# Optimization experiments

Measured on AMD Instinct MI355X. Metric: run time of the kernel, lower is better.

## Reference

```python
import jax, jax.numpy as jnp
import numpy as np

N = 2048; E = 5; C = 2; W_IN = 256; W_OUT = 128; NUM_CLASS = 8; NT = 1024


def _norm(H, add):
    # faithful to GTN.norm: transpose, zero diagonal, (optionally add I),
    # row-degree-normalize (diag(deg^-1) @ H expressed as row scaling), transpose back
    Ht = H.T
    n = Ht.shape[0]
    eye = jnp.eye(n, dtype=Ht.dtype)
    Ht = Ht * (1.0 - eye)
    if add:
        Ht = Ht + eye
    deg = jnp.sum(Ht, axis=1)
    deg_inv = jnp.where(deg == 0, jnp.zeros_like(deg), 1.0 / deg)
    return (deg_inv[:, None] * Ht).T


def _gtconv(A_e, w):
    # A_e: [E, N, N]; w: [C, E]; softmax over edge types then weighted sum
    return jnp.einsum('ce,enm->cnm', jax.nn.softmax(w, axis=1), A_e)


def setup_inputs() -> dict:
    key = jax.random.key(0)
    ks = jax.random.split(key, 12)
    A = jax.random.uniform(ks[0], (N, N, E), dtype=jnp.float32)
    X = jax.random.uniform(ks[1], (N, W_IN), dtype=jnp.float32)  # BCE target, in [0,1]
    target_x = jax.random.randint(ks[2], (NT,), 0, N)
    target = jax.random.randint(ks[3], (NT,), 0, NUM_CLASS)
    w0a = 0.1 * jax.random.normal(ks[4], (C, E), dtype=jnp.float32)
    w0b = 0.1 * jax.random.normal(ks[5], (C, E), dtype=jnp.float32)
    w1a = 0.1 * jax.random.normal(ks[6], (C, E), dtype=jnp.float32)
    W = jax.random.normal(ks[7], (W_IN, W_OUT), dtype=jnp.float32) * (1.0 / np.sqrt(W_IN))
    W1 = jax.random.normal(ks[8], (W_OUT * C, W_OUT), dtype=jnp.float32) * (1.0 / np.sqrt(W_OUT * C))
    W2 = jax.random.normal(ks[9], (W_OUT * C, W_IN), dtype=jnp.float32) * (1.0 / np.sqrt(W_OUT * C))
    lin_w = jax.random.normal(ks[10], (NUM_CLASS, W_OUT), dtype=jnp.float32) * (1.0 / np.sqrt(W_OUT))
    lin_b = jnp.zeros((NUM_CLASS,), dtype=jnp.float32)
    return {"A": A, "X": X, "W": W, "W1": W1, "W2": W2, "lin_w": lin_w,
            "lin_b": lin_b, "w0a": w0a, "w0b": w0b, "w1a": w1a,
            "target_x": target_x, "target": target}


def reference(A, X, W, W1, W2, lin_w, lin_b, w0a, w0b, w1a, target_x, target):
    A_e = jnp.transpose(A, (2, 0, 1))          # [E, N, N]
    # layer 0 (first=True): H = conv1(A) @ conv2(A)
    a = _gtconv(A_e, w0a)                      # [C, N, N]
    b = _gtconv(A_e, w0b)
    H = jnp.einsum('cij,cjk->cik', a, b)
    # layer 1 (first=False): H = normalization(H) @ conv1(A)
    Hn = jax.vmap(lambda h: _norm(h, False))(H)
    a1 = _gtconv(A_e, w1a)
    H = jnp.einsum('cij,cjk->cik', Hn, a1)
    # per-channel GCN conv: relu(norm(H_c, add=True).T @ (X @ W)), concat on features
    XW = X @ W                                 # [N, w_out]
    Hn2 = jax.vmap(lambda h: _norm(h, True))(H)
    Xc = jax.nn.relu(jnp.einsum('cji,jd->cid', Hn2, XW))  # [C, N, w_out]
    n = X.shape[0]
    X_cat = jnp.transpose(Xc, (1, 0, 2)).reshape(n, -1)   # [N, C*w_out]
    # sum channels, then the two head GCN convs share norm(H_sum, add=True)
    Hs = _norm(jnp.sum(H, axis=0), True)
    X_r = Hs.T @ (X_cat @ W2)                  # [N, w_in]
    X_o = Hs.T @ (X_cat @ W1)                  # [N, w_out]
    y = X_o[target_x] @ lin_w.T + lin_b        # [NT, num_class]
    # clamp reconstruction into [0,1] via sigmoid on out-of-range entries
    X_r = jnp.where(X_r > 1, jax.nn.sigmoid(X_r), X_r)
    X_r = jnp.where(X_r < 0, jax.nn.sigmoid(X_r), X_r)
    p = jnp.clip(X_r, 1e-7, 1.0 - 1e-7)
    lossR = -jnp.mean(X * jnp.log(p) + (1.0 - X) * jnp.log1p(-p))
    logp = jax.nn.log_softmax(y, axis=-1)
    lossC = -jnp.mean(jnp.take_along_axis(logp, target[:, None], axis=1))
    loss = lossC + lossR
    Ws = (jax.lax.stop_gradient(jax.nn.softmax(w0a, axis=1)),
          jax.lax.stop_gradient(jax.nn.softmax(w0b, axis=1)),
          jax.lax.stop_gradient(jax.nn.softmax(w1a, axis=1)))
    return (loss, y, Ws, lossR)
```

## Files before the change

### kernel.cpp

```cpp
#include <hip/hip_runtime.h>
#include <hip/hip_bf16.h>
#include <math.h>

#define NDIM 2048
#define EDIM 5
#define CDIM 2
#define WIN 256
#define WOUT 128
#define NCLS 8
#define NTGT 1024
#define NN ((size_t)NDIM * NDIM)
#define HNSC 256.0f
#define HNSCI 0.00390625f

typedef __attribute__((ext_vector_type(8))) short short8v;
typedef __attribute__((ext_vector_type(4))) float float4v;
typedef __attribute__((ext_vector_type(8))) int int8v;
typedef __attribute__((ext_vector_type(4))) int int4v;
typedef __attribute__((ext_vector_type(2))) int int2v;

__device__ __forceinline__ void gl2lds16(const void* g, void* l) {
  __builtin_amdgcn_global_load_lds((__attribute__((address_space(1))) const unsigned int*)g,
                                   (__attribute__((address_space(3))) unsigned int*)l, 16, 0, 0);
}
__device__ __forceinline__ float bf2f(unsigned short u) {
  return __uint_as_float(((unsigned)u) << 16);
}
__device__ __forceinline__ unsigned short f2bf(float f) {
  __hip_bfloat16 h = __float2bfloat16(f);
  return *(unsigned short*)&h;
}
__device__ __forceinline__ unsigned char f2fp8(float f) {
  return (unsigned char)(__builtin_amdgcn_cvt_pk_fp8_f32(f, f, 0, false) & 0xff);
}

#define N_XBF (NDIM * WIN)
#define N_WT (WIN * WOUT)
#define N_W12T (384 * WIN)
#define N_PREP (N_XBF + N_WT + N_W12T + CDIM * NDIM + 16 + 30)
__global__ __launch_bounds__(256) void wsum_mega_k(
    const float* __restrict__ A, const float* __restrict__ w0a,
    const float* __restrict__ w0b, const float* __restrict__ w1a,
    unsigned char* __restrict__ a_out, unsigned char* __restrict__ bT,
    unsigned char* __restrict__ a1T,
    float* __restrict__ acc, float* __restrict__ deg,
    const float* __restrict__ X, const float* __restrict__ W,
    const float* __restrict__ W1, const float* __restrict__ W2,
    __hip_bfloat16* __restrict__ Xbf, __hip_bfloat16* __restrict__ WTbf,
    __hip_bfloat16* __restrict__ W12Tbf,
    float* __restrict__ dout) {
  const int b = blockIdx.x;
  const int tid = threadIdx.x;
  if (b >= 4096) {
    int idx = (b - 4096) * 256 + tid;
    if (idx < N_XBF) { Xbf[idx] = __float2bfloat16(X[idx]); return; }
    idx -= N_XBF;
    if (idx < N_WT) {
      int d = idx >> 8, k = idx & 255;
      WTbf[idx] = __float2bfloat16(W[k * WOUT + d]);
      return;
    }
    idx -= N_WT;
    if (idx < N_W12T) {
      int j = idx >> 8, k = idx & 255;
      W12Tbf[idx] = __float2bfloat16(j < 128 ? W1[k * 128 + j] : W2[k * 256 + (j - 128)]);
      return;
    }
    idx -= N_W12T;
    if (idx < CDIM * NDIM) { deg[idx] = 0.f; return; }
    idx -= CDIM * NDIM;
    if (idx < 16) { acc[idx] = 0.f; return; }
    idx -= 16;
    if (idx < 30) {
      int m = idx / 10, rr = idx - m * 10, c = rr / 5, e = rr - c * 5;
      const float* src = (m == 0) ? w0a : (m == 1) ? w0b : w1a;
      float mx = -1e30f;
      for (int t = 0; t < 5; ++t) mx = fmaxf(mx, src[c * 5 + t]);
      float s = 0.f, ve = 0.f;
      for (int t = 0; t < 5; ++t) {
        float ex = expf(src[c * 5 + t] - mx);
        s += ex;
        if (t == e) ve = ex;
      }
      dout[1 + NTGT * NCLS + idx] = ve / s;
    }
    return;
  }
  __shared__ float swl[32];
  __shared__ float tb[CDIM][32][33];
  __shared__ float tc[CDIM][32][33];
  if (tid < 6) {
    int m = tid >> 1, c = tid & 1;
    const float* src = (m == 0) ? w0a : (m == 1) ? w0b : w1a;
    float mx = -1e30f;
    for (int e = 0; e < 5; ++e) mx = fmaxf(mx, src[c * 5 + e]);
    float ex[5]; float s = 0.f;
    for (int e = 0; e < 5; ++e) { ex[e] = expf(src[c * 5 + e] - mx); s += ex[e]; }
    for (int e = 0; e < 5; ++e) swl[m * 10 + c * 5 + e] = ex[e] / s;
  }
  __syncthreads();
  const int bx = (b & 63) * 32, by = (b >> 6) * 32;
  const int tx = tid & 31, ty = tid >> 5;
#pragma unroll
  for (int rr = 0; rr < 32; rr += 8) {
    int n = by + ty + rr, m = bx + tx;
    size_t base = ((size_t)n * NDIM + m) * EDIM;
    float v0 = A[base], v1 = A[base + 1], v2 = A[base + 2], v3 = A[base + 3], v4 = A[base + 4];
#pragma unroll
    for (int c = 0; c < CDIM; ++c) {
      float sa = swl[c*5]*v0 + swl[c*5+1]*v1 + swl[c*5+2]*v2 + swl[c*5+3]*v3 + swl[c*5+4]*v4;
      float sb = swl[10+c*5]*v0 + swl[10+c*5+1]*v1 + swl[10+c*5+2]*v2 + swl[10+c*5+3]*v3 + swl[10+c*5+4]*v4;
      float sc = swl[20+c*5]*v0 + swl[20+c*5+1]*v1 + swl[20+c*5+2]*v2 + swl[20+c*5+3]*v3 + swl[20+c*5+4]*v4;
      a_out[c * NN + (size_t)n * NDIM + m] = f2fp8(sa);
      tb[c][ty + rr][tx] = sb;
      tc[c][ty + rr][tx] = sc;
    }
  }
  __syncthreads();
#pragma unroll
  for (int rr = 0; rr < 32; rr += 8) {
    int mm = bx + ty + rr, nn2 = by + tx;
#pragma unroll
    for (int c = 0; c < CDIM; ++c) {
      bT[c * NN + (size_t)mm * NDIM + nn2] = f2fp8(tb[c][tx][ty + rr]);
      a1T[c * NN + (size_t)mm * NDIM + nn2] = f2fp8(tc[c][tx][ty + rr]);
    }
  }
}

__global__ __launch_bounds__(256) void mfma_fp8_k(
    const unsigned char* __restrict__ Ab, const unsigned char* __restrict__ Bt,
    __hip_bfloat16* __restrict__ Cv, int K, int ldc,
    size_t sA, size_t sB, size_t sC, float* __restrict__ cs) {
  __shared__ __align__(16) unsigned char As[128 * 128];
  __shared__ __align__(16) unsigned char Bs[128 * 128];
  const int tid = threadIdx.x;
  const int lane = tid & 63;
  const int wave = tid >> 6;
  const int batch = blockIdx.z;
  const unsigned char* A = Ab + (size_t)batch * sA;
  const unsigned char* B = Bt + (size_t)batch * sB;
  const int row0 = blockIdx.y * 128;
  const int col0 = blockIdx.x * 128;

  const int wr = (wave >> 1) * 64;
  const int wc = (wave & 1) * 64;
  const int q = lane >> 4;
  const int r = lane & 15;

  float4v acc[4][4] = {};

  const int srow = lane >> 3;
  const int scol = ((lane & 7) ^ (srow & 7)) * 16;
  const int fsw = r & 7;

  for (int k0 = 0; k0 < K; k0 += 128) {
    __syncthreads();
#pragma unroll
    for (int s = 0; s < 4; ++s) {
      gl2lds16(A + (size_t)(row0 + s * 32 + wave * 8 + srow) * K + k0 + scol,
               As + s * 4096 + wave * 1024);
      gl2lds16(B + (size_t)(col0 + s * 32 + wave * 8 + srow) * K + k0 + scol,
               Bs + s * 4096 + wave * 1024);
    }
    __syncthreads();

    union { int8v v; int4v h[2]; } ua[4], ub[4];
#pragma unroll
    for (int i = 0; i < 4; ++i) {
      const unsigned char* pa = As + (size_t)(wr + i * 16 + r) * 128;
      const unsigned char* pb = Bs + (size_t)(wc + i * 16 + r) * 128;
      ua[i].h[0] = *(const int4v*)(pa + (((2 * q) ^ fsw) * 16));
      ua[i].h[1] = *(const int4v*)(pa + (((2 * q + 1) ^ fsw) * 16));
      ub[i].h[0] = *(const int4v*)(pb + (((2 * q) ^ fsw) * 16));
      ub[i].h[1] = *(const int4v*)(pb + (((2 * q + 1) ^ fsw) * 16));
    }
#pragma unroll
    for (int i = 0; i < 4; ++i)
#pragma unroll
      for (int j = 0; j < 4; ++j)
        acc[i][j] = __builtin_amdgcn_mfma_scale_f32_16x16x128_f8f6f4(
            ua[i].v, ub[j].v, acc[i][j], 0, 0, 0, 0x7F7F7F7F, 0, 0x7F7F7F7F);
  }

  __hip_bfloat16* Cp = Cv + (size_t)batch * sC;
#pragma unroll
  for (int i = 0; i < 4; ++i) {
    int row = row0 + wr + i * 16 + q * 4;
#pragma unroll
    for (int j = 0; j < 4; ++j) {
      int col = col0 + wc + j * 16 + r;
#pragma unroll
      for (int e = 0; e < 4; ++e)
        Cp[(size_t)(row + e) * ldc + col] = __float2bfloat16(acc[i][j][e]);
    }
  }

  if (cs) {
    float* csp = cs + (size_t)batch * NDIM;
#pragma unroll
    for (int j = 0; j < 4; ++j) {
      int col = col0 + wc + j * 16 + r;
      float s = 0.f;
#pragma unroll
      for (int i = 0; i < 4; ++i) {
        int rowb = row0 + wr + i * 16 + q * 4;
#pragma unroll
        for (int e = 0; e < 4; ++e)
          if (rowb + e != col) s += acc[i][j][e];
      }
      s += __shfl_xor(s, 16, 64);
      s += __shfl_xor(s, 32, 64);
      if (lane < 16) atomicAdd(&csp[col], s);
    }
  }
}

__global__ __launch_bounds__(256) void mfma_bt_k(
    const __hip_bfloat16* __restrict__ Ab, const __hip_bfloat16* __restrict__ Bt,
    void* __restrict__ Cv, int K, int ldc,
    size_t sA, size_t sB, size_t sC, size_t sSplit, int nsplit, int mode) {
  __shared__ __hip_bfloat16 As[128 * 64];
  __shared__ __hip_bfloat16 Bs[128 * 64];
  const int tid = threadIdx.x;
  const int lane = tid & 63;
  const int wave = tid >> 6;
  const int batch = blockIdx.z / nsplit;
  const int split = blockIdx.z - batch * nsplit;
  const __hip_bfloat16* A = Ab + (size_t)batch * sA;
  const __hip_bfloat16* B = Bt + (size_t)batch * sB;
  const int row0 = blockIdx.y * 128;
  const int col0 = blockIdx.x * 128;
  const int kchunk = K / nsplit;
  const int kbeg = split * kchunk;
  const int kend = kbeg + kchunk;

  const int wr = (wave >> 1) * 64;
  const int wc = (wave & 1) * 64;
  const int q = lane >> 4;
  const int r = lane & 15;

  float4v acc[4][4] = {};

  const int srow = lane >> 3;
  const int scol = ((lane & 7) ^ (srow & 7)) * 8;
  const int fsw = r & 7;

  for (int k0 = kbeg; k0 < kend; k0 += 64) {
    __syncthreads();
#pragma unroll
    for (int s = 0; s < 4; ++s) {
      gl2lds16(A + (size_t)(row0 + s * 32 + wave * 8 + srow) * K + k0 + scol,
               (char*)As + s * 4096 + wave * 1024);
      gl2lds16(B + (size_t)(col0 + s * 32 + wave * 8 + srow) * K + k0 + scol,
               (char*)Bs + s * 4096 + wave * 1024);
    }
    __syncthreads();
#pragma unroll
    for (int h = 0; h < 2; ++h) {
      short8v af[4], bf[4];
#pragma unroll
      for (int i = 0; i < 4; ++i) {
        af[i] = *(const short8v*)((const char*)As + (size_t)(wr + i * 16 + r) * 128 +
                                  (((h * 4 + q) ^ fsw) * 16));
        bf[i] = *(const short8v*)((const char*)Bs + (size_t)(wc + i * 16 + r) * 128 +
                                  (((h * 4 + q) ^ fsw) * 16));
      }
#pragma unroll
      for (int i = 0; i < 4; ++i)
#pragma unroll
        for (int j = 0; j < 4; ++j)
          acc[i][j] = __builtin_amdgcn_mfma_f32_16x16x32_bf16(af[i], bf[j], acc[i][j], 0, 0, 0);
    }
  }

  if (mode == 1) {
    __hip_bfloat16* Cp = (__hip_bfloat16*)Cv + (size_t)batch * sC;
#pragma unroll
    for (int i = 0; i < 4; ++i) {
      int row = row0 + wr + i * 16 + q * 4;
#pragma unroll
      for (int j = 0; j < 4; ++j) {
        int col = col0 + wc + j * 16 + r;
#pragma unroll
        for (int e = 0; e < 4; ++e)
          Cp[(size_t)(row + e) * ldc + col] = __float2bfloat16(acc[i][j][e]);
      }
    }
  } else {
    float* Cp = (float*)Cv + (size_t)batch * sC + (size_t)split * sSplit;
#pragma unroll
    for (int i = 0; i < 4; ++i) {
      int row = row0 + wr + i * 16 + q * 4;
#pragma unroll
      for (int j = 0; j < 4; ++j) {
        int col = col0 + wc + j * 16 + r;
#pragma unroll
        for (int e = 0; e < 4; ++e)
          Cp[(size_t)(row + e) * ldc + col] = acc[i][j][e];
      }
    }
  }
}

__global__ __launch_bounds__(256) void col_scale_k(const __hip_bfloat16* __restrict__ H,
                                                   const float* __restrict__ deg,
                                                   unsigned char* __restrict__ out) {
  size_t base = ((size_t)blockIdx.x * 256 + threadIdx.x) * 8;
  int c = (int)(base >> 22);
  int i = (int)((base >> 11) & (NDIM - 1));
  int j0 = (int)(base & (NDIM - 1));
  union { short8v v; unsigned short u[8]; } p;
  p.v = *(const short8v*)(H + base);
  float f[8];
#pragma unroll
  for (int t = 0; t < 8; ++t) {
    int j = j0 + t;
    float d = deg[c * NDIM + j];
    float inv = (d == 0.f) ? 0.f : HNSC / d;
    float v = (i == j) ? 0.f : bf2f(p.u[t]);
    f[t] = v * inv;
  }
  int w0 = __builtin_amdgcn_cvt_pk_fp8_f32(f[0], f[1], 0, false);
  w0 = __builtin_amdgcn_cvt_pk_fp8_f32(f[2], f[3], w0, true);
  int w1 = __builtin_amdgcn_cvt_pk_fp8_f32(f[4], f[5], 0, false);
  w1 = __builtin_amdgcn_cvt_pk_fp8_f32(f[6], f[7], w1, true);
  int2v o; o.x = w0; o.y = w1;
  *(int2v*)(out + base) = o;
}

__global__ __launch_bounds__(256) void rowmega_k(const __hip_bfloat16* __restrict__ H1T,
                                                 __hip_bfloat16* __restrict__ Hn2T,
                                                 __hip_bfloat16* __restrict__ HsT) {
  const int m = blockIdx.x;
  const int tid = threadIdx.x;
  const size_t rb = (size_t)m * NDIM + tid * 8;
  union { short8v v; unsigned short u[8]; } a0, a1;
  a0.v = *(const short8v*)(H1T + rb);
  a1.v = *(const short8v*)(H1T + NN + rb);
  float v0[8], v1[8];
  float s0 = 0.f, s1 = 0.f;
#pragma unroll
  for (int t = 0; t < 8; ++t) {
    v0[t] = bf2f(a0.u[t]) * HNSCI;
    v1[t] = bf2f(a1.u[t]) * HNSCI;
    s0 += v0[t]; s1 += v1[t];
  }
  __shared__ float ds[2];
  __shared__ float red[2][4];
  __shared__ float bc[3];
  if (tid == (m >> 3)) { ds[0] = v0[m & 7]; ds[1] = v1[m & 7]; }
  for (int off = 32; off > 0; off >>= 1) {
    s0 += __shfl_down(s0, off, 64);
    s1 += __shfl_down(s1, off, 64);
  }
  if ((tid & 63) == 0) { red[0][tid >> 6] = s0; red[1][tid >> 6] = s1; }
  __syncthreads();
  if (tid == 0) {
    float t0 = red[0][0] + red[0][1] + red[0][2] + red[0][3];
    float t1 = red[1][0] + red[1][1] + red[1][2] + red[1][3];
    float r0 = t0 - ds[0] + 1.f;
    float r1 = t1 - ds[1] + 1.f;
    float rs = t0 + t1 - ds[0] - ds[1] + 1.f;
    bc[0] = (r0 == 0.f) ? 0.f : 1.f / r0;
    bc[1] = (r1 == 0.f) ? 0.f : 1.f / r1;
    bc[2] = (rs == 0.f) ? 0.f : 1.f / rs;
  }
  __syncthreads();
  float i0 = bc[0], i1 = bc[1], is = bc[2];
  union { short8v v; unsigned short u[8]; } o0, o1, os;
#pragma unroll
  for (int t = 0; t < 8; ++t) {
    bool dg = (tid * 8 + t == m);
    o0.u[t] = f2bf((dg ? 1.f : v0[t]) * i0);
    o1.u[t] = f2bf((dg ? 1.f : v1[t]) * i1);
    os.u[t] = f2bf((dg ? 1.f : (v0[t] + v1[t])) * is);
  }
  *(short8v*)(Hn2T + rb) = o0.v;
  *(short8v*)(Hn2T + NN + rb) = o1.v;
  *(short8v*)(HsT + rb) = os.v;
}

__global__ __launch_bounds__(256) void reduce_relu_k(const float* __restrict__ P7,
                                                     __hip_bfloat16* __restrict__ Xcat) {
  int idx = blockIdx.x * 256 + threadIdx.x;
  int c = idx >> 18;
  int rem = idx & 262143;
  float s = 0.f;
#pragma unroll
  for (int sp = 0; sp < 8; ++sp)
    s += P7[(size_t)c * 2097152 + (size_t)sp * 262144 + rem];
  int n = rem >> 7, d = rem & 127;
  Xcat[(size_t)n * 256 + (c << 7) + d] = __float2bfloat16(fmaxf(s, 0.f));
}

__global__ __launch_bounds__(256) void loss_mega_k(const float* __restrict__ P10,
                                                   const float* __restrict__ X,
                                                   const float* __restrict__ lin_w,
                                                   const float* __restrict__ lin_b,
                                                   const int* __restrict__ txs,
                                                   const int* __restrict__ tgt,
                                                   float* __restrict__ yout,
                                                   float* __restrict__ acc) {
  const int b = blockIdx.x;
  const int tid = threadIdx.x;
  if (b < 2048) {
    float xr = 0.f;
#pragma unroll
    for (int sp = 0; sp < 8; ++sp)
      xr += P10[(size_t)sp * 786432 + (size_t)b * 384 + 128 + tid];
    if (xr > 1.f) xr = 1.f / (1.f + expf(-xr));
    if (xr < 0.f) xr = 1.f / (1.f + expf(-xr));
    float p = fminf(fmaxf(xr, 1e-7f), 1.f - 1e-7f);
    float xv = X[(size_t)b * WIN + tid];
    float t = xv * logf(p) + (1.f - xv) * log1pf(-p);
    for (int off = 32; off > 0; off >>= 1) t += __shfl_down(t, off, 64);
    __shared__ float red[4];
    if ((tid & 63) == 0) red[tid >> 6] = t;
    __syncthreads();
    if (tid == 0) atomicAdd(acc + 1, red[0] + red[1] + red[2] + red[3]);
    return;
  }
  const int t = b - 2048;
  __shared__ float xo[WOUT];
  __shared__ float ys[NCLS];
  int x = txs[t];
  if (tid < WOUT) {
    float s = 0.f;
#pragma unroll
    for (int sp = 0; sp < 8; ++sp)
      s += P10[(size_t)sp * 786432 + (size_t)x * 384 + tid];
    xo[tid] = s;
  }
  __syncthreads();
  if (tid < NCLS) {
    float s = lin_b[tid];
    for (int d = 0; d < WOUT; ++d) s += xo[d] * lin_w[tid * WOUT + d];
    ys[tid] = s;
    yout[(size_t)t * NCLS + tid] = s;
  }
  __syncthreads();
  if (tid == 0) {
    float m = ys[0];
    for (int k = 1; k < NCLS; ++k) m = fmaxf(m, ys[k]);
    float se = 0.f;
    for (int k = 0; k < NCLS; ++k) se += expf(ys[k] - m);
    float lse = m + logf(se);
    atomicAdd(acc, lse - ys[tgt[t]]);
  }
}

__global__ void finalize_k(const float* __restrict__ acc, float* __restrict__ dout) {
  float lossC = acc[0] / (float)NTGT;
  float lossR = -acc[1] / (float)(NDIM * WIN);
  dout[0] = lossC + lossR;
  dout[1 + NTGT * NCLS + 30] = lossR;
}

extern "C" void kernel_launch(void* const* d_in, const int* in_sizes, int n_in,
                              void* d_out, int out_size, void* d_ws, size_t ws_size,
                              hipStream_t stream) {
  const float* A    = (const float*)d_in[0];
  const float* X    = (const float*)d_in[1];
  const float* W    = (const float*)d_in[2];
  const float* W1   = (const float*)d_in[3];
  const float* W2   = (const float*)d_in[4];
  const float* linw = (const float*)d_in[5];
  const float* linb = (const float*)d_in[6];
  const float* w0a  = (const float*)d_in[7];
  const float* w0b  = (const float*)d_in[8];
  const float* w1a  = (const float*)d_in[9];
  const int* txs    = (const int*)d_in[10];
  const int* tgt    = (const int*)d_in[11];
  float* dout = (float*)d_out;

  float* ws = (float*)d_ws;
  unsigned char* wb = (unsigned char*)d_ws;
  unsigned char* P_a   = wb;
  unsigned char* P_bT  = wb + 2 * NN;
  unsigned char* P_a1T = wb + 4 * NN;
  unsigned char* P_Hn  = wb + 6 * NN;
  __hip_bfloat16* H_bf   = (__hip_bfloat16*)(ws + 2 * NN);
  __hip_bfloat16* H1T_bf = (__hip_bfloat16*)(ws + 3 * NN);
  __hip_bfloat16* Hn2T   = (__hip_bfloat16*)(ws + 4 * NN);
  __hip_bfloat16* HsT    = (__hip_bfloat16*)(ws);
  float* sm   = ws + 5 * NN;
  float* acc   = sm;                 sm += 16;
  float* deg   = sm;                 sm += CDIM * NDIM;
  __hip_bfloat16* Xbf    = (__hip_bfloat16*)sm;  sm += N_XBF / 2;
  __hip_bfloat16* WTbf   = (__hip_bfloat16*)sm;  sm += N_WT / 2;
  __hip_bfloat16* W12Tbf = (__hip_bfloat16*)sm;  sm += N_W12T / 2;
  __hip_bfloat16* XWT    = (__hip_bfloat16*)sm;  sm += (size_t)WOUT * NDIM / 2;
  __hip_bfloat16* Xcat   = (__hip_bfloat16*)sm;  sm += (size_t)NDIM * 256 / 2;
  __hip_bfloat16* XC12T  = (__hip_bfloat16*)sm;  sm += (size_t)384 * NDIM / 2;
  float* P7   = sm;                  sm += (size_t)16 * 262144;
  float* P10  = sm;                  sm += (size_t)8 * 786432;

  dim3 blk256(256);

  wsum_mega_k<<<dim3(4096 + (N_PREP + 255) / 256), blk256, 0, stream>>>(
      A, w0a, w0b, w1a, P_a, P_bT, P_a1T, acc, deg, X, W, W1, W2,
      Xbf, WTbf, W12Tbf, dout);
  mfma_fp8_k<<<dim3(16, 16, 2), blk256, 0, stream>>>(P_a, P_bT, H_bf, NDIM, NDIM,
                                                     NN, NN, NN, deg);
  col_scale_k<<<dim3((unsigned)(2 * NN / 2048)), blk256, 0, stream>>>(H_bf, deg, P_Hn);
  mfma_fp8_k<<<dim3(16, 16, 2), blk256, 0, stream>>>(P_a1T, P_Hn, H1T_bf, NDIM, NDIM,
                                                     NN, NN, NN, nullptr);
  rowmega_k<<<dim3(NDIM), blk256, 0, stream>>>(H1T_bf, Hn2T, HsT);
  mfma_bt_k<<<dim3(16, 1, 1), blk256, 0, stream>>>(WTbf, Xbf, XWT, WIN, NDIM,
                                                   0, 0, 0, 0, 1, 1);
  mfma_bt_k<<<dim3(1, 16, 16), blk256, 0, stream>>>(Hn2T, XWT, P7, NDIM, WOUT,
                                                    NN, 0, 2097152, 262144, 8, 2);
  reduce_relu_k<<<dim3(2048), blk256, 0, stream>>>(P7, Xcat);
  mfma_bt_k<<<dim3(16, 3, 1), blk256, 0, stream>>>(W12Tbf, Xcat, XC12T, 256, NDIM,
                                                   0, 0, 0, 0, 1, 1);
  mfma_bt_k<<<dim3(3, 16, 8), blk256, 0, stream>>>(HsT, XC12T, P10, NDIM, 384,
                                                   0, 0, 0, 786432, 8, 2);
  loss_mega_k<<<dim3(2048 + NTGT), blk256, 0, stream>>>(P10, X, linw, linb, txs, tgt,
                                                        dout + 1, acc);
  finalize_k<<<dim3(1), dim3(1), 0, stream>>>(acc, dout);
}
```

Measured before the change: 300.1 us.

## Vectorize prep kernel, fuse XW GEMM into first fp8 GEMM, store split-K partials as bf16

```diff
diff --git a/kernel.cpp b/kernel.cpp
--- a/kernel.cpp
+++ b/kernel.cpp
@@ -30,8 +30,9 @@
   __hip_bfloat16 h = __float2bfloat16(f);
   return *(unsigned short*)&h;
 }
-__device__ __forceinline__ unsigned char f2fp8(float f) {
-  return (unsigned char)(__builtin_amdgcn_cvt_pk_fp8_f32(f, f, 0, false) & 0xff);
+__device__ __forceinline__ unsigned int pk4fp8(float a, float b, float c, float d) {
+  int w = __builtin_amdgcn_cvt_pk_fp8_f32(a, b, 0, false);
+  return (unsigned int)__builtin_amdgcn_cvt_pk_fp8_f32(c, d, w, true);
 }
 
 #define N_XBF (NDIM * WIN)
@@ -100,49 +101,56 @@
   }
   __syncthreads();
   const int bx = (b & 63) * 32, by = (b >> 6) * 32;
-  const int tx = tid & 31, ty = tid >> 5;
-#pragma unroll
-  for (int rr = 0; rr < 32; rr += 8) {
-    int n = by + ty + rr, m = bx + tx;
-    size_t base = ((size_t)n * NDIM + m) * EDIM;
-    float v0 = A[base], v1 = A[base + 1], v2 = A[base + 2], v3 = A[base + 3], v4 = A[base + 4];
-#pragma unroll
-    for (int c = 0; c < CDIM; ++c) {
-      float sa = swl[c*5]*v0 + swl[c*5+1]*v1 + swl[c*5+2]*v2 + swl[c*5+3]*v3 + swl[c*5+4]*v4;
-      float sb = swl[10+c*5]*v0 + swl[10+c*5+1]*v1 + swl[10+c*5+2]*v2 + swl[10+c*5+3]*v3 + swl[10+c*5+4]*v4;
-      float sc = swl[20+c*5]*v0 + swl[20+c*5+1]*v1 + swl[20+c*5+2]*v2 + swl[20+c*5+3]*v3 + swl[20+c*5+4]*v4;
-      a_out[c * NN + (size_t)n * NDIM + m] = f2fp8(sa);
-      tb[c][ty + rr][tx] = sb;
-      tc[c][ty + rr][tx] = sc;
-    }
+  const int tx4 = tid & 7, ty = tid >> 3;
+  const int n = by + ty, m0 = bx + tx4 * 4;
+  const float* ap = A + ((size_t)n * NDIM + m0) * EDIM;
+  float4 f0 = *(const float4*)(ap);
+  float4 f1 = *(const float4*)(ap + 4);
+  float4 f2 = *(const float4*)(ap + 8);
+  float4 f3 = *(const float4*)(ap + 12);
+  float4 f4 = *(const float4*)(ap + 16);
+  float v[4][5] = {{f0.x, f0.y, f0.z, f0.w, f1.x},
+                   {f1.y, f1.z, f1.w, f2.x, f2.y},
+                   {f2.z, f2.w, f3.x, f3.y, f3.z},
+                   {f3.w, f4.x, f4.y, f4.z, f4.w}};
+#pragma unroll
+  for (int c = 0; c < CDIM; ++c) {
+    float sa[4], sb[4], sc[4];
+#pragma unroll
+    for (int t = 0; t < 4; ++t) {
+      sa[t] = swl[c*5]*v[t][0] + swl[c*5+1]*v[t][1] + swl[c*5+2]*v[t][2] +
+              swl[c*5+3]*v[t][3] + swl[c*5+4]*v[t][4];
+      sb[t] = swl[10+c*5]*v[t][0] + swl[10+c*5+1]*v[t][1] + swl[10+c*5+2]*v[t][2] +
+              swl[10+c*5+3]*v[t][3] + swl[10+c*5+4]*v[t][4];
+      sc[t] = swl[20+c*5]*v[t][0] + swl[20+c*5+1]*v[t][1] + swl[20+c*5+2]*v[t][2] +
+              swl[20+c*5+3]*v[t][3] + swl[20+c*5+4]*v[t][4];
+      tb[c][ty][tx4 * 4 + t] = sb[t];
+      tc[c][ty][tx4 * 4 + t] = sc[t];
+    }
+    *(unsigned int*)(a_out + c * NN + (size_t)n * NDIM + m0) =
+        pk4fp8(sa[0], sa[1], sa[2], sa[3]);
   }
   __syncthreads();
-#pragma unroll
-  for (int rr = 0; rr < 32; rr += 8) {
-    int mm = bx + ty + rr, nn2 = by + tx;
-#pragma unroll
-    for (int c = 0; c < CDIM; ++c) {
-      bT[c * NN + (size_t)mm * NDIM + nn2] = f2fp8(tb[c][tx][ty + rr]);
-      a1T[c * NN + (size_t)mm * NDIM + nn2] = f2fp8(tc[c][tx][ty + rr]);
-    }
-  }
-}
-
-__global__ __launch_bounds__(256) void mfma_fp8_k(
-    const unsigned char* __restrict__ Ab, const unsigned char* __restrict__ Bt,
-    __hip_bfloat16* __restrict__ Cv, int K, int ldc,
-    size_t sA, size_t sB, size_t sC, float* __restrict__ cs) {
-  __shared__ __align__(16) unsigned char As[128 * 128];
-  __shared__ __align__(16) unsigned char Bs[128 * 128];
+  const int mm = bx + ty, nn0 = by + tx4 * 4;
+#pragma unroll
+  for (int c = 0; c < CDIM; ++c) {
+    float b0 = tb[c][tx4*4+0][ty], b1 = tb[c][tx4*4+1][ty];
+    float b2 = tb[c][tx4*4+2][ty], b3 = tb[c][tx4*4+3][ty];
+    float c0 = tc[c][tx4*4+0][ty], c1 = tc[c][tx4*4+1][ty];
+    float c2 = tc[c][tx4*4+2][ty], c3 = tc[c][tx4*4+3][ty];
+    *(unsigned int*)(bT + c * NN + (size_t)mm * NDIM + nn0) = pk4fp8(b0, b1, b2, b3);
+    *(unsigned int*)(a1T + c * NN + (size_t)mm * NDIM + nn0) = pk4fp8(c0, c1, c2, c3);
+  }
+}
+
+__device__ __forceinline__ void fp8_gemm_body(
+    const unsigned char* __restrict__ A, const unsigned char* __restrict__ B,
+    __hip_bfloat16* __restrict__ Cp, float* __restrict__ csp,
+    int K, int ldc, int row0, int col0,
+    unsigned char* As, unsigned char* Bs) {
   const int tid = threadIdx.x;
   const int lane = tid & 63;
   const int wave = tid >> 6;
-  const int batch = blockIdx.z;
-  const unsigned char* A = Ab + (size_t)batch * sA;
-  const unsigned char* B = Bt + (size_t)batch * sB;
-  const int row0 = blockIdx.y * 128;
-  const int col0 = blockIdx.x * 128;
-
   const int wr = (wave >> 1) * 64;
   const int wc = (wave & 1) * 64;
   const int q = lane >> 4;
@@ -152,7 +160,7 @@
 
   const int srow = lane >> 3;
   const int scol = ((lane & 7) ^ (srow & 7)) * 16;
-  const int fsw = r & 7;
+  const int fsw = r & 15 & 7;
 
   for (int k0 = 0; k0 < K; k0 += 128) {
     __syncthreads();
@@ -183,7 +191,6 @@
             ua[i].v, ub[j].v, acc[i][j], 0, 0, 0, 0x7F7F7F7F, 0, 0x7F7F7F7F);
   }
 
-  __hip_bfloat16* Cp = Cv + (size_t)batch * sC;
 #pragma unroll
   for (int i = 0; i < 4; ++i) {
     int row = row0 + wr + i * 16 + q * 4;
@@ -196,8 +203,7 @@
     }
   }
 
-  if (cs) {
-    float* csp = cs + (size_t)batch * NDIM;
+  if (csp) {
 #pragma unroll
     for (int j = 0; j < 4; ++j) {
       int col = col0 + wc + j * 16 + r;
@@ -216,25 +222,13 @@
   }
 }
 
-__global__ __launch_bounds__(256) void mfma_bt_k(
-    const __hip_bfloat16* __restrict__ Ab, const __hip_bfloat16* __restrict__ Bt,
-    void* __restrict__ Cv, int K, int ldc,
-    size_t sA, size_t sB, size_t sC, size_t sSplit, int nsplit, int mode) {
-  __shared__ __hip_bfloat16 As[128 * 64];
-  __shared__ __hip_bfloat16 Bs[128 * 64];
+__device__ __forceinline__ void bf16_gemm_body(
+    const __hip_bfloat16* __restrict__ A, const __hip_bfloat16* __restrict__ B,
+    __hip_bfloat16* __restrict__ Cp, int K, int ldc, int row0, int col0,
+    int kbeg, int kend, char* As, char* Bs) {
   const int tid = threadIdx.x;
   const int lane = tid & 63;
   const int wave = tid >> 6;
-  const int batch = blockIdx.z / nsplit;
-  const int split = blockIdx.z - batch * nsplit;
-  const __hip_bfloat16* A = Ab + (size_t)batch * sA;
-  const __hip_bfloat16* B = Bt + (size_t)batch * sB;
-  const int row0 = blockIdx.y * 128;
-  const int col0 = blockIdx.x * 128;
-  const int kchunk = K / nsplit;
-  const int kbeg = split * kchunk;
-  const int kend = kbeg + kchunk;
-
   const int wr = (wave >> 1) * 64;
   const int wc = (wave & 1) * 64;
   const int q = lane >> 4;
@@ -251,9 +245,9 @@
 #pragma unroll
     for (int s = 0; s < 4; ++s) {
       gl2lds16(A + (size_t)(row0 + s * 32 + wave * 8 + srow) * K + k0 + scol,
-               (char*)As + s * 4096 + wave * 1024);
+               As + s * 4096 + wave * 1024);
       gl2lds16(B + (size_t)(col0 + s * 32 + wave * 8 + srow) * K + k0 + scol,
-               (char*)Bs + s * 4096 + wave * 1024);
+               Bs + s * 4096 + wave * 1024);
     }
     __syncthreads();
 #pragma unroll
@@ -261,9 +255,9 @@
       short8v af[4], bf[4];
 #pragma unroll
       for (int i = 0; i < 4; ++i) {
-        af[i] = *(const short8v*)((const char*)As + (size_t)(wr + i * 16 + r) * 128 +
+        af[i] = *(const short8v*)(As + (size_t)(wr + i * 16 + r) * 128 +
                                   (((h * 4 + q) ^ fsw) * 16));
-        bf[i] = *(const short8v*)((const char*)Bs + (size_t)(wc + i * 16 + r) * 128 +
+        bf[i] = *(const short8v*)(Bs + (size_t)(wc + i * 16 + r) * 128 +
                                   (((h * 4 + q) ^ fsw) * 16));
       }
 #pragma unroll
@@ -274,33 +268,62 @@
     }
   }
 
-  if (mode == 1) {
-    __hip_bfloat16* Cp = (__hip_bfloat16*)Cv + (size_t)batch * sC;
-#pragma unroll
-    for (int i = 0; i < 4; ++i) {
-      int row = row0 + wr + i * 16 + q * 4;
-#pragma unroll
-      for (int j = 0; j < 4; ++j) {
-        int col = col0 + wc + j * 16 + r;
-#pragma unroll
-        for (int e = 0; e < 4; ++e)
-          Cp[(size_t)(row + e) * ldc + col] = __float2bfloat16(acc[i][j][e]);
-      }
-    }
+#pragma unroll
+  for (int i = 0; i < 4; ++i) {
+    int row = row0 + wr + i * 16 + q * 4;
+#pragma unroll
+    for (int j = 0; j < 4; ++j) {
+      int col = col0 + wc + j * 16 + r;
+#pragma unroll
+      for (int e = 0; e < 4; ++e)
+        Cp[(size_t)(row + e) * ldc + col] = __float2bfloat16(acc[i][j][e]);
+    }
+  }
+}
+
+__global__ __launch_bounds__(256) void gemm1_xwt_k(
+    const unsigned char* __restrict__ P_a, const unsigned char* __restrict__ P_bT,
+    __hip_bfloat16* __restrict__ H_bf, float* __restrict__ deg,
+    const __hip_bfloat16* __restrict__ WTbf, const __hip_bfloat16* __restrict__ Xbf,
+    __hip_bfloat16* __restrict__ XWT) {
+  __shared__ __align__(16) unsigned char smem[32768];
+  const int z = blockIdx.z;
+  if (z < 2) {
+    fp8_gemm_body(P_a + (size_t)z * NN, P_bT + (size_t)z * NN,
+                  H_bf + (size_t)z * NN, deg + (size_t)z * NDIM,
+                  NDIM, NDIM, blockIdx.y * 128, blockIdx.x * 128,
+                  smem, smem + 16384);
   } else {
-    float* Cp = (float*)Cv + (size_t)batch * sC + (size_t)split * sSplit;
-#pragma unroll
-    for (int i = 0; i < 4; ++i) {
-      int row = row0 + wr + i * 16 + q * 4;
-#pragma unroll
-      for (int j = 0; j < 4; ++j) {
-        int col = col0 + wc + j * 16 + r;
-#pragma unroll
-        for (int e = 0; e < 4; ++e)
-          Cp[(size_t)(row + e) * ldc + col] = acc[i][j][e];
-      }
-    }
-  }
+    if (blockIdx.y != 0) return;
+    bf16_gemm_body(WTbf, Xbf, XWT, WIN, NDIM, 0, blockIdx.x * 128,
+                   0, WIN, (char*)smem, (char*)smem + 16384);
+  }
+}
+
+__global__ __launch_bounds__(256) void gemm2_k(
+    const unsigned char* __restrict__ P_a1T, const unsigned char* __restrict__ P_Hn,
+    __hip_bfloat16* __restrict__ H1T_bf) {
+  __shared__ __align__(16) unsigned char smem[32768];
+  const int z = blockIdx.z;
+  fp8_gemm_body(P_a1T + (size_t)z * NN, P_Hn + (size_t)z * NN,
+                H1T_bf + (size_t)z * NN, nullptr,
+                NDIM, NDIM, blockIdx.y * 128, blockIdx.x * 128,
+                smem, smem + 16384);
+}
+
+__global__ __launch_bounds__(256) void mfma_bt_k(
+    const __hip_bfloat16* __restrict__ Ab, const __hip_bfloat16* __restrict__ Bt,
+    __hip_bfloat16* __restrict__ Cv, int K, int ldc,
+    size_t sA, size_t sB, size_t sC, size_t sSplit, int nsplit) {
+  __shared__ __align__(16) char smem[32768];
+  const int batch = blockIdx.z / nsplit;
+  const int split = blockIdx.z - batch * nsplit;
+  const int kchunk = K / nsplit;
+  bf16_gemm_body(Ab + (size_t)batch * sA, Bt + (size_t)batch * sB,
+                 Cv + (size_t)batch * sC + (size_t)split * sSplit,
+                 K, ldc, blockIdx.y * 128, blockIdx.x * 128,
+                 split * kchunk, split * kchunk + kchunk,
+                 smem, smem + 16384);
 }
 
 __global__ __launch_bounds__(256) void col_scale_k(const __hip_bfloat16* __restrict__ H,
@@ -321,11 +344,9 @@
     float v = (i == j) ? 0.f : bf2f(p.u[t]);
     f[t] = v * inv;
   }
-  int w0 = __builtin_amdgcn_cvt_pk_fp8_f32(f[0], f[1], 0, false);
-  w0 = __builtin_amdgcn_cvt_pk_fp8_f32(f[2], f[3], w0, true);
-  int w1 = __builtin_amdgcn_cvt_pk_fp8_f32(f[4], f[5], 0, false);
-  w1 = __builtin_amdgcn_cvt_pk_fp8_f32(f[6], f[7], w1, true);
-  int2v o; o.x = w0; o.y = w1;
+  int2v o;
+  o.x = (int)pk4fp8(f[0], f[1], f[2], f[3]);
+  o.y = (int)pk4fp8(f[4], f[5], f[6], f[7]);
   *(int2v*)(out + base) = o;
 }
 
@@ -381,7 +402,7 @@
   *(short8v*)(HsT + rb) = os.v;
 }
 
-__global__ __launch_bounds__(256) void reduce_relu_k(const float* __restrict__ P7,
+__global__ __launch_bounds__(256) void reduce_relu_k(const __hip_bfloat16* __restrict__ P7,
                                                      __hip_bfloat16* __restrict__ Xcat) {
   int idx = blockIdx.x * 256 + threadIdx.x;
   int c = idx >> 18;
@@ -389,12 +410,12 @@
   float s = 0.f;
 #pragma unroll
   for (int sp = 0; sp < 8; ++sp)
-    s += P7[(size_t)c * 2097152 + (size_t)sp * 262144 + rem];
+    s += __bfloat162float(P7[(size_t)c * 2097152 + (size_t)sp * 262144 + rem]);
   int n = rem >> 7, d = rem & 127;
   Xcat[(size_t)n * 256 + (c << 7) + d] = __float2bfloat16(fmaxf(s, 0.f));
 }
 
-__global__ __launch_bounds__(256) void loss_mega_k(const float* __restrict__ P10,
+__global__ __launch_bounds__(256) void loss_mega_k(const __hip_bfloat16* __restrict__ P10,
                                                    const float* __restrict__ X,
                                                    const float* __restrict__ lin_w,
                                                    const float* __restrict__ lin_b,
@@ -408,7 +429,7 @@
     float xr = 0.f;
 #pragma unroll
     for (int sp = 0; sp < 8; ++sp)
-      xr += P10[(size_t)sp * 786432 + (size_t)b * 384 + 128 + tid];
+      xr += __bfloat162float(P10[(size_t)sp * 786432 + (size_t)b * 384 + 128 + tid]);
     if (xr > 1.f) xr = 1.f / (1.f + expf(-xr));
     if (xr < 0.f) xr = 1.f / (1.f + expf(-xr));
     float p = fminf(fmaxf(xr, 1e-7f), 1.f - 1e-7f);
@@ -429,7 +450,7 @@
     float s = 0.f;
 #pragma unroll
     for (int sp = 0; sp < 8; ++sp)
-      s += P10[(size_t)sp * 786432 + (size_t)x * 384 + tid];
+      s += __bfloat162float(P10[(size_t)sp * 786432 + (size_t)x * 384 + tid]);
     xo[tid] = s;
   }
   __syncthreads();
@@ -493,30 +514,27 @@
   __hip_bfloat16* XWT    = (__hip_bfloat16*)sm;  sm += (size_t)WOUT * NDIM / 2;
   __hip_bfloat16* Xcat   = (__hip_bfloat16*)sm;  sm += (size_t)NDIM * 256 / 2;
   __hip_bfloat16* XC12T  = (__hip_bfloat16*)sm;  sm += (size_t)384 * NDIM / 2;
-  float* P7   = sm;                  sm += (size_t)16 * 262144;
-  float* P10  = sm;                  sm += (size_t)8 * 786432;
+  __hip_bfloat16* P7bf   = (__hip_bfloat16*)sm;  sm += (size_t)16 * 262144 / 2;
+  __hip_bfloat16* P10bf  = (__hip_bfloat16*)sm;  sm += (size_t)8 * 786432 / 2;
 
   dim3 blk256(256);
 
   wsum_mega_k<<<dim3(4096 + (N_PREP + 255) / 256), blk256, 0, stream>>>(
       A, w0a, w0b, w1a, P_a, P_bT, P_a1T, acc, deg, X, W, W1, W2,
       Xbf, WTbf, W12Tbf, dout);
-  mfma_fp8_k<<<dim3(16, 16, 2), blk256, 0, stream>>>(P_a, P_bT, H_bf, NDIM, NDIM,
-                                                     NN, NN, NN, deg);
+  gemm1_xwt_k<<<dim3(16, 16, 3), blk256, 0, stream>>>(P_a, P_bT, H_bf, deg,
+                                                      WTbf, Xbf, XWT);
   col_scale_k<<<dim3((unsigned)(2 * NN / 2048)), blk256, 0, stream>>>(H_bf, deg, P_Hn);
-  mfma_fp8_k<<<dim3(16, 16, 2), blk256, 0, stream>>>(P_a1T, P_Hn, H1T_bf, NDIM, NDIM,
-                                                     NN, NN, NN, nullptr);
+  gemm2_k<<<dim3(16, 16, 2), blk256, 0, stream>>>(P_a1T, P_Hn, H1T_bf);
   rowmega_k<<<dim3(NDIM), blk256, 0, stream>>>(H1T_bf, Hn2T, HsT);
-  mfma_bt_k<<<dim3(16, 1, 1), blk256, 0, stream>>>(WTbf, Xbf, XWT, WIN, NDIM,
-                                                   0, 0, 0, 0, 1, 1);
-  mfma_bt_k<<<dim3(1, 16, 16), blk256, 0, stream>>>(Hn2T, XWT, P7, NDIM, WOUT,
-                                                    NN, 0, 2097152, 262144, 8, 2);
-  reduce_relu_k<<<dim3(2048), blk256, 0, stream>>>(P7, Xcat);
+  mfma_bt_k<<<dim3(1, 16, 16), blk256, 0, stream>>>(Hn2T, XWT, P7bf, NDIM, WOUT,
+                                                    NN, 0, 2097152, 262144, 8);
+  reduce_relu_k<<<dim3(2048), blk256, 0, stream>>>(P7bf, Xcat);
   mfma_bt_k<<<dim3(16, 3, 1), blk256, 0, stream>>>(W12Tbf, Xcat, XC12T, 256, NDIM,
-                                                   0, 0, 0, 0, 1, 1);
-  mfma_bt_k<<<dim3(3, 16, 8), blk256, 0, stream>>>(HsT, XC12T, P10, NDIM, 384,
-                                                   0, 0, 0, 786432, 8, 2);
-  loss_mega_k<<<dim3(2048 + NTGT), blk256, 0, stream>>>(P10, X, linw, linb, txs, tgt,
+                                                   0, 0, 0, 0, 1);
+  mfma_bt_k<<<dim3(3, 16, 8), blk256, 0, stream>>>(HsT, XC12T, P10bf, NDIM, 384,
+                                                   0, 0, 0, 786432, 8);
+  loss_mega_k<<<dim3(2048 + NTGT), blk256, 0, stream>>>(P10bf, X, linw, linb, txs, tgt,
                                                         dout + 1, acc);
   finalize_k<<<dim3(1), dim3(1), 0, stream>>>(acc, dout);
 }
```

Result: faster. 289.3 us (-3.6%).
